# Performance work log

Hardware: AMD Instinct MI355X
Metric: run time of the kernel (lower is better)

## Reference

```python
import jax, jax.numpy as jnp
import numpy as np

N_NODES = 100000
N_EDGES = 3200000


def setup_inputs() -> dict:
    key = jax.random.key(0)
    ks = jax.random.split(key, 8)
    x = jax.random.normal(ks[0], (N_NODES, 128), dtype=jnp.float32)
    edge_index = jax.random.randint(ks[1], (2, N_EDGES), 0, N_NODES, dtype=jnp.int64)
    edge_weight = jax.random.uniform(ks[2], (N_EDGES,), dtype=jnp.float32)
    W1 = jax.random.normal(ks[3], (128, 32), dtype=jnp.float32) * (1.0 / np.sqrt(128))
    b1 = jnp.zeros((32,), dtype=jnp.float32)
    W2 = jax.random.normal(ks[4], (32, 16), dtype=jnp.float32) * (1.0 / np.sqrt(32))
    b2 = jnp.zeros((16,), dtype=jnp.float32)
    Wfc = jax.random.normal(ks[5], (16, 1), dtype=jnp.float32) * (1.0 / np.sqrt(16))
    bfc = jnp.zeros((1,), dtype=jnp.float32)
    return {"x": x, "edge_index": edge_index, "edge_weight": edge_weight,
            "W1": W1, "b1": b1, "W2": W2, "b2": b2, "Wfc": Wfc, "bfc": bfc}


def _gcn_norm(edge_index, edge_weight, num_nodes):
    # PyG gcn_norm: add self-loops (weight 1), sym-normalize by in-degree of target (col)
    row, col = edge_index[0], edge_index[1]
    loop = jnp.arange(num_nodes, dtype=row.dtype)
    row_f = jnp.concatenate([row, loop])
    col_f = jnp.concatenate([col, loop])
    w_f = jnp.concatenate([edge_weight, jnp.ones((num_nodes,), edge_weight.dtype)])
    deg = jax.ops.segment_sum(w_f, col_f, num_segments=num_nodes)
    dinv = jnp.where(deg > 0, deg ** -0.5, 0.0)
    norm_w = dinv[row_f] * w_f * dinv[col_f]  # [E+N]
    return row_f, col_f, norm_w


def _gcn_conv(x, row_f, col_f, norm_w, W, b, num_nodes):
    h = x @ W                      # transform first (in->out dims)
    msg = h[row_f] * norm_w[:, None]  # gather source features, scale by edge norm
    out = jax.ops.segment_sum(msg, col_f, num_segments=num_nodes)  # scatter-add to targets
    return out + b


def reference(x, edge_index, edge_weight, W1, b1, W2, b2, Wfc, bfc):
    N = x.shape[0]
    row_f, col_f, norm_w = _gcn_norm(edge_index, edge_weight, N)
    h = jax.nn.leaky_relu(_gcn_conv(x, row_f, col_f, norm_w, W1, b1, N))
    # dropout is identity in eval mode; norm=False skips GraphNorm
    h = jax.nn.leaky_relu(_gcn_conv(h, row_f, col_f, norm_w, W2, b2, N))
    return h @ Wfc + bfc  # [N, 1]
```

## Files before the change

### kernel.cpp

```cpp
#include <hip/hip_runtime.h>
#include <hip/hip_fp16.h>

#define N_NODES 100000
#define N_EDGES 3200000
#define BSHIFT 7
#define BSIZE 128
#define NB ((N_NODES + BSIZE - 1) / BSIZE)
#define CAP 4736
#define ROWBITS 17
#define ROWMASK ((1 << ROWBITS) - 1)
#define EB2 ((N_EDGES + 2047) / 2048)


__global__ void k_detect(const unsigned* __restrict__ w, int* __restrict__ flag) {
    __shared__ unsigned s[256];
    unsigned v = 0;
    for (int t = threadIdx.x; t < 4096; t += 256) v |= w[2 * t + 1];
    s[threadIdx.x] = v;
    __syncthreads();
    for (int off = 128; off > 0; off >>= 1) {
        if (threadIdx.x < (unsigned)off) s[threadIdx.x] |= s[threadIdx.x + off];
        __syncthreads();
    }
    if (threadIdx.x == 0) flag[0] = (s[0] == 0) ? 1 : 0;
}

__device__ __forceinline__ void load_edge(const unsigned* __restrict__ e, int f, int E,
                                          int i, int& r, int& c) {
    if (f) { r = (int)e[2 * i]; c = (int)e[2 * E + 2 * i]; }
    else   { r = (int)e[i];     c = (int)e[E + i]; }
}


__global__ __launch_bounds__(256) void k_scatter(const unsigned* __restrict__ eidx,
                                                 const int* __restrict__ flag,
                                                 const float* __restrict__ ew,
                                                 int* __restrict__ gcursor,
                                                 int2* __restrict__ bstage, int E, int n) {
    __shared__ int lcnt[NB];
    __shared__ int lbase[NB];
    __shared__ int lcur[NB];
    int tid = threadIdx.x;
    for (int i = tid; i < NB; i += 256) { lcnt[i] = 0; lcur[i] = 0; }
    __syncthreads();
    int f = flag[0];
    int base = blockIdx.x * 2048;
    int rr[8], cc[8];
    float wv[8];
#pragma unroll
    for (int i = 0; i < 8; ++i) {
        int e = base + i * 256 + tid;
        rr[i] = -1; cc[i] = 0; wv[i] = 0.f;
        if (e < E) {
            int r, c;
            load_edge(eidx, f, E, e, r, c);
            if ((unsigned)r < (unsigned)n && (unsigned)c < (unsigned)n) {
                rr[i] = r; cc[i] = c; wv[i] = ew[e];
            }
        }
    }
#pragma unroll
    for (int i = 0; i < 8; ++i)
        if (rr[i] >= 0) atomicAdd(&lcnt[cc[i] >> BSHIFT], 1);
    __syncthreads();
    for (int i = tid; i < NB; i += 256)
        if (lcnt[i]) lbase[i] = atomicAdd(&gcursor[i], lcnt[i]);
    __syncthreads();
#pragma unroll
    for (int i = 0; i < 8; ++i) {
        if (rr[i] >= 0) {
            int b = cc[i] >> BSHIFT, off = cc[i] & (BSIZE - 1);
            int pos = lbase[b] + atomicAdd(&lcur[b], 1);
            if (pos < CAP)
                bstage[(size_t)b * CAP + pos] =
                    make_int2((off << ROWBITS) | rr[i], __float_as_int(wv[i]));
        }
    }
}


__global__ __launch_bounds__(256) void k_passb(const int* __restrict__ gcursor,
                                               int2* __restrict__ erw,
                                               int* __restrict__ start,
                                               int* __restrict__ end,
                                               float* __restrict__ dinv, int n) {
    __shared__ int2  se[CAP];
    __shared__ int   cnt[256];
    __shared__ float wsm[BSIZE];
    __shared__ int   cur[BSIZE];
    int tid = threadIdx.x;
    int b = blockIdx.x;
    int n0 = b << BSHIFT;
    int nn = min(BSIZE, n - n0);
    size_t bb = (size_t)b * CAP;
    int cntE = min(gcursor[b], CAP);
    cnt[tid] = 0;
    if (tid < BSIZE) wsm[tid] = 0.f;
    __syncthreads();
    for (int e = tid; e < cntE; e += 256) {
        int2 kv = erw[bb + e];
        se[e] = kv;
        int off = kv.x >> ROWBITS;
        atomicAdd(&cnt[off], 1);
        atomicAdd(&wsm[off], __int_as_float(kv.y));
    }
    __syncthreads();
    int v = cnt[tid];
    for (int o = 1; o < 256; o <<= 1) {
        int t = (tid >= o) ? cnt[tid - o] : 0;
        __syncthreads();
        cnt[tid] += t;
        __syncthreads();
    }
    int excl = cnt[tid] - v;
    if (tid < nn) {
        start[n0 + tid] = (int)bb + excl;
        end[n0 + tid]   = (int)bb + excl + v;
        dinv[n0 + tid]  = 1.0f / sqrtf(1.0f + wsm[tid]);
    }
    if (tid < BSIZE) cur[tid] = excl;
    __syncthreads();
    for (int e = tid; e < cntE; e += 256) {
        int2 kv = se[e];
        int off = kv.x >> ROWBITS;
        int p = atomicAdd(&cur[off], 1);
        erw[bb + p] = make_int2(kv.x & ROWMASK, kv.y);
    }
}


__global__ __launch_bounds__(256) void k_gemm1(const float* __restrict__ x,
                                               const float* __restrict__ W1,
                                               const float* __restrict__ dinv,
                                               __half* __restrict__ g1, int n) {
    __shared__ float W1s[128 * 32];
    __shared__ float xs[8][128];
    int tid = threadIdx.x;
    for (int i = tid; i < 1024; i += 256)
        *reinterpret_cast<float4*>(W1s + 4 * i) = reinterpret_cast<const float4*>(W1)[i];
    int node0 = blockIdx.x * 8;
    {
        int ln = tid >> 5, ii = tid & 31;
        int node = node0 + ln;
        float4 vv = make_float4(0.f, 0.f, 0.f, 0.f);
        if (node < n) vv = reinterpret_cast<const float4*>(x)[node * 32 + ii];
        *reinterpret_cast<float4*>(&xs[ln][4 * ii]) = vv;
    }
    __syncthreads();
    int ln = tid >> 5;
    int kk = tid & 31;
    int node = node0 + ln;
    if (node < n) {
        float acc = 0.f;
#pragma unroll
        for (int i = 0; i < 128; ++i) acc += xs[ln][i] * W1s[i * 32 + kk];
        g1[node * 32 + kk] = __float2half(dinv[node] * acc);
    }
}


__global__ __launch_bounds__(256) void k_agg1(const __half* __restrict__ g,
                                              const int* __restrict__ start,
                                              const int* __restrict__ end,
                                              const int2* __restrict__ erw,
                                              const float* __restrict__ dinv,
                                              const float* __restrict__ b1,
                                              float* __restrict__ h, int n) {
    int wid = (blockIdx.x * 256 + threadIdx.x) >> 6;
    int l = threadIdx.x & 63;
    if (wid >= n) return;
    int slot = l >> 3;
    int cg   = l & 7;
    int s = start[wid], en = end[wid];
    float4 acc = make_float4(0.f, 0.f, 0.f, 0.f);
    for (int e0 = s; e0 < en; e0 += 8) {
        int e = e0 + slot;
        if (e < en) {
            int2 rw = erw[e];
            float w = __int_as_float(rw.y);
            float2 raw = *reinterpret_cast<const float2*>(g + ((size_t)rw.x << 5) + (cg << 2));
            __half2 h01 = *reinterpret_cast<const __half2*>(&raw.x);
            __half2 h23 = *reinterpret_cast<const __half2*>(&raw.y);
            float2 f01 = __half22float2(h01), f23 = __half22float2(h23);
            acc.x += w * f01.x; acc.y += w * f01.y;
            acc.z += w * f23.x; acc.w += w * f23.y;
        }
    }
#pragma unroll
    for (int m = 8; m <= 32; m <<= 1) {
        acc.x += __shfl_xor(acc.x, m);
        acc.y += __shfl_xor(acc.y, m);
        acc.z += __shfl_xor(acc.z, m);
        acc.w += __shfl_xor(acc.w, m);
    }
    if (slot == 0) {
        float2 raw = *reinterpret_cast<const float2*>(g + ((size_t)wid << 5) + (cg << 2));
        __half2 h01 = *reinterpret_cast<const __half2*>(&raw.x);
        __half2 h23 = *reinterpret_cast<const __half2*>(&raw.y);
        float2 f01 = __half22float2(h01), f23 = __half22float2(h23);
        float di = dinv[wid];
        float4 b = *reinterpret_cast<const float4*>(b1 + (cg << 2));
        float4 v;
        v.x = di * (acc.x + f01.x) + b.x;
        v.y = di * (acc.y + f01.y) + b.y;
        v.z = di * (acc.z + f23.x) + b.z;
        v.w = di * (acc.w + f23.y) + b.w;
        v.x = v.x > 0.f ? v.x : 0.01f * v.x;
        v.y = v.y > 0.f ? v.y : 0.01f * v.y;
        v.z = v.z > 0.f ? v.z : 0.01f * v.z;
        v.w = v.w > 0.f ? v.w : 0.01f * v.w;
        *reinterpret_cast<float4*>(h + ((size_t)wid << 5) + (cg << 2)) = v;
    }
}


__global__ __launch_bounds__(256) void k_gemm2(const float* __restrict__ h1,
                                               const float* __restrict__ W2,
                                               const float* __restrict__ dinv,
                                               __half* __restrict__ g2, int n) {
    __shared__ float W2s[32 * 16];
    int tid = threadIdx.x;
    for (int i = tid; i < 32 * 16; i += 256) W2s[i] = W2[i];
    __syncthreads();
    int t = blockIdx.x * 256 + tid;
    if (t < n * 16) {
        int node = t >> 4, j = t & 15;
        float acc = 0.f;
#pragma unroll
        for (int k = 0; k < 32; ++k) acc += h1[node * 32 + k] * W2s[k * 16 + j];
        g2[t] = __float2half(dinv[node] * acc);
    }
}


__global__ __launch_bounds__(256) void k_agg2(const __half* __restrict__ g2,
                                              const int* __restrict__ start,
                                              const int* __restrict__ end,
                                              const int2* __restrict__ erw,
                                              const float* __restrict__ dinv,
                                              const float* __restrict__ b2,
                                              const float* __restrict__ Wfc,
                                              const float* __restrict__ bfc,
                                              float* __restrict__ out, int n) {
    int wid = (blockIdx.x * 256 + threadIdx.x) >> 6;
    int l = threadIdx.x & 63;
    if (wid >= n) return;
    int slot = l >> 2;
    int cg   = l & 3;
    int s = start[wid], en = end[wid];
    float4 acc = make_float4(0.f, 0.f, 0.f, 0.f);
    for (int e0 = s; e0 < en; e0 += 16) {
        int e = e0 + slot;
        if (e < en) {
            int2 rw = erw[e];
            float w = __int_as_float(rw.y);
            float2 raw = *reinterpret_cast<const float2*>(g2 + ((size_t)rw.x << 4) + (cg << 2));
            __half2 h01 = *reinterpret_cast<const __half2*>(&raw.x);
            __half2 h23 = *reinterpret_cast<const __half2*>(&raw.y);
            float2 f01 = __half22float2(h01), f23 = __half22float2(h23);
            acc.x += w * f01.x; acc.y += w * f01.y;
            acc.z += w * f23.x; acc.w += w * f23.y;
        }
    }
#pragma unroll
    for (int m = 4; m <= 32; m <<= 1) {
        acc.x += __shfl_xor(acc.x, m);
        acc.y += __shfl_xor(acc.y, m);
        acc.z += __shfl_xor(acc.z, m);
        acc.w += __shfl_xor(acc.w, m);
    }
    float2 raw = *reinterpret_cast<const float2*>(g2 + ((size_t)wid << 4) + (cg << 2));
    __half2 h01 = *reinterpret_cast<const __half2*>(&raw.x);
    __half2 h23 = *reinterpret_cast<const __half2*>(&raw.y);
    float2 f01 = __half22float2(h01), f23 = __half22float2(h23);
    float di = dinv[wid];
    float4 b = *reinterpret_cast<const float4*>(b2 + (cg << 2));
    float4 wf = *reinterpret_cast<const float4*>(Wfc + (cg << 2));
    float4 v;
    v.x = di * (acc.x + f01.x) + b.x;
    v.y = di * (acc.y + f01.y) + b.y;
    v.z = di * (acc.z + f23.x) + b.z;
    v.w = di * (acc.w + f23.y) + b.w;
    v.x = v.x > 0.f ? v.x : 0.01f * v.x;
    v.y = v.y > 0.f ? v.y : 0.01f * v.y;
    v.z = v.z > 0.f ? v.z : 0.01f * v.z;
    v.w = v.w > 0.f ? v.w : 0.01f * v.w;
    float p = v.x * wf.x + v.y * wf.y + v.z * wf.z + v.w * wf.w;
    p += __shfl_xor(p, 1);
    p += __shfl_xor(p, 2);
    if (l == 0) out[wid] = p + bfc[0];
}

extern "C" void kernel_launch(void* const* d_in, const int* in_sizes, int n_in,
                              void* d_out, int out_size, void* d_ws, size_t ws_size,
                              hipStream_t stream) {
    const float*    x    = (const float*)d_in[0];
    const unsigned* eidx = (const unsigned*)d_in[1];
    const float*    ew   = (const float*)d_in[2];
    const float*    W1   = (const float*)d_in[3];
    const float*    b1   = (const float*)d_in[4];
    const float*    W2   = (const float*)d_in[5];
    const float*    b2   = (const float*)d_in[6];
    const float*    Wfc  = (const float*)d_in[7];
    const float*    bfc  = (const float*)d_in[8];
    float* out = (float*)d_out;

    const int N = N_NODES;
    const int E = N_EDGES;

    char* ws = (char*)d_ws;
    int*    flag    = (int*)ws;
    int*    gcursor = (int*)(ws + 4096);
    int*    start   = (int*)(ws + 64u * 1024);
    int*    end     = (int*)(ws + 512u * 1024);
    float*  dinv    = (float*)(ws + 1024u * 1024);
    int2*   erw     = (int2*)(ws + 2u * 1024 * 1024);
    __half* g1h     = (__half*)(ws + 32u * 1024 * 1024);
    float*  h1      = (float*)(ws + 39u * 1024 * 1024);
    __half* g2h     = (__half*)(ws + 52u * 1024 * 1024);

    k_detect<<<1, 256, 0, stream>>>(eidx, flag);

    hipMemsetAsync(gcursor, 0, (size_t)NB * sizeof(int), stream);
    k_scatter<<<EB2, 256, 0, stream>>>(eidx, flag, ew, gcursor, erw, E, N);
    k_passb<<<NB, 256, 0, stream>>>(gcursor, erw, start, end, dinv, N);

    k_gemm1<<<(N + 7) / 8, 256, 0, stream>>>(x, W1, dinv, g1h, N);
    {
        int blocks = (int)(((long long)N * 64 + 255) / 256);
        k_agg1<<<blocks, 256, 0, stream>>>(g1h, start, end, erw, dinv, b1, h1, N);
    }

    k_gemm2<<<(N * 16 + 255) / 256, 256, 0, stream>>>(h1, W2, dinv, g2h, N);
    {
        int blocks = (int)(((long long)N * 64 + 255) / 256);
        k_agg2<<<blocks, 256, 0, stream>>>(g2h, start, end, erw, dinv, b2, Wfc, bfc, out, N);
    }
}
```

Measured before the change: 373.2 us.

## Enlarge scatter chunks to cut global cursor atomics; branchless aggregation loops

The edge bucketing kernel now has 512-thread blocks each handle 8192 edges instead of 2048. Edges are loaded twice from global memory, once to count and once to place, rather than held in registers. This reduces the number of global cursor atomics and the staging fragmentation per bucket, at the cost of re-reading the edge arrays. Both aggregation kernels also remove the per-edge branch by clamping the index and zeroing the weight, which keeps lanes converged but issues some redundant gathers on the tail iteration.

```diff
diff --git a/kernel.cpp b/kernel.cpp
--- a/kernel.cpp
+++ b/kernel.cpp
@@ -9,7 +9,8 @@
 #define CAP 4736
 #define ROWBITS 17
 #define ROWMASK ((1 << ROWBITS) - 1)
-#define EB2 ((N_EDGES + 2047) / 2048)
+#define EPB 8192
+#define SC_GRID ((N_EDGES + EPB - 1) / EPB)
 
 
 __global__ void k_detect(const unsigned* __restrict__ w, int* __restrict__ flag) {
@@ -32,48 +33,39 @@
 }
 
 
-__global__ __launch_bounds__(256) void k_scatter(const unsigned* __restrict__ eidx,
+__global__ __launch_bounds__(512) void k_scatter(const unsigned* __restrict__ eidx,
                                                  const int* __restrict__ flag,
                                                  const float* __restrict__ ew,
                                                  int* __restrict__ gcursor,
                                                  int2* __restrict__ bstage, int E, int n) {
     __shared__ int lcnt[NB];
     __shared__ int lbase[NB];
-    __shared__ int lcur[NB];
     int tid = threadIdx.x;
-    for (int i = tid; i < NB; i += 256) { lcnt[i] = 0; lcur[i] = 0; }
+    for (int i = tid; i < NB; i += 512) lcnt[i] = 0;
     __syncthreads();
     int f = flag[0];
-    int base = blockIdx.x * 2048;
-    int rr[8], cc[8];
-    float wv[8];
-#pragma unroll
-    for (int i = 0; i < 8; ++i) {
-        int e = base + i * 256 + tid;
-        rr[i] = -1; cc[i] = 0; wv[i] = 0.f;
-        if (e < E) {
-            int r, c;
-            load_edge(eidx, f, E, e, r, c);
-            if ((unsigned)r < (unsigned)n && (unsigned)c < (unsigned)n) {
-                rr[i] = r; cc[i] = c; wv[i] = ew[e];
-            }
-        }
-    }
-#pragma unroll
-    for (int i = 0; i < 8; ++i)
-        if (rr[i] >= 0) atomicAdd(&lcnt[cc[i] >> BSHIFT], 1);
-    __syncthreads();
-    for (int i = tid; i < NB; i += 256)
+    int base = blockIdx.x * EPB;
+    int lim = min(EPB, E - base);
+    for (int i = tid; i < lim; i += 512) {
+        int r, c;
+        load_edge(eidx, f, E, base + i, r, c);
+        if ((unsigned)r < (unsigned)n && (unsigned)c < (unsigned)n)
+            atomicAdd(&lcnt[c >> BSHIFT], 1);
+    }
+    __syncthreads();
+    for (int i = tid; i < NB; i += 512)
         if (lcnt[i]) lbase[i] = atomicAdd(&gcursor[i], lcnt[i]);
     __syncthreads();
-#pragma unroll
-    for (int i = 0; i < 8; ++i) {
-        if (rr[i] >= 0) {
-            int b = cc[i] >> BSHIFT, off = cc[i] & (BSIZE - 1);
-            int pos = lbase[b] + atomicAdd(&lcur[b], 1);
+    for (int i = tid; i < lim; i += 512) {
+        int e = base + i;
+        int r, c;
+        load_edge(eidx, f, E, e, r, c);
+        if ((unsigned)r < (unsigned)n && (unsigned)c < (unsigned)n) {
+            int b = c >> BSHIFT, off = c & (BSIZE - 1);
+            int pos = atomicAdd(&lbase[b], 1);
             if (pos < CAP)
                 bstage[(size_t)b * CAP + pos] =
-                    make_int2((off << ROWBITS) | rr[i], __float_as_int(wv[i]));
+                    make_int2((off << ROWBITS) | r, __float_as_int(ew[e]));
         }
     }
 }
@@ -175,16 +167,15 @@
     float4 acc = make_float4(0.f, 0.f, 0.f, 0.f);
     for (int e0 = s; e0 < en; e0 += 8) {
         int e = e0 + slot;
-        if (e < en) {
-            int2 rw = erw[e];
-            float w = __int_as_float(rw.y);
-            float2 raw = *reinterpret_cast<const float2*>(g + ((size_t)rw.x << 5) + (cg << 2));
-            __half2 h01 = *reinterpret_cast<const __half2*>(&raw.x);
-            __half2 h23 = *reinterpret_cast<const __half2*>(&raw.y);
-            float2 f01 = __half22float2(h01), f23 = __half22float2(h23);
-            acc.x += w * f01.x; acc.y += w * f01.y;
-            acc.z += w * f23.x; acc.w += w * f23.y;
-        }
+        bool ok = e < en;
+        int2 rw = erw[ok ? e : s];
+        float w = ok ? __int_as_float(rw.y) : 0.f;
+        float2 raw = *reinterpret_cast<const float2*>(g + ((size_t)rw.x << 5) + (cg << 2));
+        __half2 h01 = *reinterpret_cast<const __half2*>(&raw.x);
+        __half2 h23 = *reinterpret_cast<const __half2*>(&raw.y);
+        float2 f01 = __half22float2(h01), f23 = __half22float2(h23);
+        acc.x += w * f01.x; acc.y += w * f01.y;
+        acc.z += w * f23.x; acc.w += w * f23.y;
     }
 #pragma unroll
     for (int m = 8; m <= 32; m <<= 1) {
@@ -251,16 +242,15 @@
     float4 acc = make_float4(0.f, 0.f, 0.f, 0.f);
     for (int e0 = s; e0 < en; e0 += 16) {
         int e = e0 + slot;
-        if (e < en) {
-            int2 rw = erw[e];
-            float w = __int_as_float(rw.y);
-            float2 raw = *reinterpret_cast<const float2*>(g2 + ((size_t)rw.x << 4) + (cg << 2));
-            __half2 h01 = *reinterpret_cast<const __half2*>(&raw.x);
-            __half2 h23 = *reinterpret_cast<const __half2*>(&raw.y);
-            float2 f01 = __half22float2(h01), f23 = __half22float2(h23);
-            acc.x += w * f01.x; acc.y += w * f01.y;
-            acc.z += w * f23.x; acc.w += w * f23.y;
-        }
+        bool ok = e < en;
+        int2 rw = erw[ok ? e : s];
+        float w = ok ? __int_as_float(rw.y) : 0.f;
+        float2 raw = *reinterpret_cast<const float2*>(g2 + ((size_t)rw.x << 4) + (cg << 2));
+        __half2 h01 = *reinterpret_cast<const __half2*>(&raw.x);
+        __half2 h23 = *reinterpret_cast<const __half2*>(&raw.y);
+        float2 f01 = __half22float2(h01), f23 = __half22float2(h23);
+        acc.x += w * f01.x; acc.y += w * f01.y;
+        acc.z += w * f23.x; acc.w += w * f23.y;
     }
 #pragma unroll
     for (int m = 4; m <= 32; m <<= 1) {
@@ -322,7 +312,7 @@
     k_detect<<<1, 256, 0, stream>>>(eidx, flag);
 
     hipMemsetAsync(gcursor, 0, (size_t)NB * sizeof(int), stream);
-    k_scatter<<<EB2, 256, 0, stream>>>(eidx, flag, ew, gcursor, erw, E, N);
+    k_scatter<<<SC_GRID, 512, 0, stream>>>(eidx, flag, ew, gcursor, erw, E, N);
     k_passb<<<NB, 256, 0, stream>>>(gcursor, erw, start, end, dinv, N);
 
     k_gemm1<<<(N + 7) / 8, 256, 0, stream>>>(x, W1, dinv, g1h, N);
```

Result: no change. 373.5 us (+0.1%).
